# Kernel tuning notes

Hardware: AMD Instinct MI355X
Metric: run time of the kernel (lower is better)

Reference implementation:

```python
import jax, jax.numpy as jnp
import numpy as np

V, E, H = 32000, 256, 512

def gru_cell(x, h, W_ih, W_hh, b_ih, b_hh):
    # PyTorch GRU cell: gates ordered (r, z, n)
    gi = x @ W_ih.T + b_ih
    gh = h @ W_hh.T + b_hh
    i_r, i_z, i_n = jnp.split(gi, 3, axis=-1)
    h_r, h_z, h_n = jnp.split(gh, 3, axis=-1)
    r = jax.nn.sigmoid(i_r + h_r)
    z = jax.nn.sigmoid(i_z + h_z)
    n = jnp.tanh(i_n + r * h_n)
    return (1.0 - z) * n + z * h


def setup_inputs() -> dict:
    key = jax.random.key(0)
    ks = jax.random.split(key, 16)
    B, Tx, Ty = 32, 512, 128
    s = lambda k, sh: jax.random.normal(k, sh, jnp.float32) * 0.05
    return {
        "x": jax.random.randint(ks[0], (B, Tx), 0, V),
        "y": jax.random.randint(ks[1], (B, Ty), 0, V),
        "embedding": s(ks[2], (V, E)),
        "enc_W_ih": s(ks[3], (3 * H, E)),
        "enc_W_hh": s(ks[4], (3 * H, H)),
        "enc_b_ih": s(ks[5], (3 * H,)),
        "enc_b_hh": s(ks[6], (3 * H,)),
        "dec_W_ih": s(ks[7], (3 * H, E + H)),
        "dec_W_hh": s(ks[8], (3 * H, H)),
        "dec_b_ih": s(ks[9], (3 * H,)),
        "dec_b_hh": s(ks[10], (3 * H,)),
        "h_init": s(ks[11], (1, H)),
        "fc_W": s(ks[12], (V, H)),
        "fc_b": s(ks[13], (V,)),
    }


def reference(x, y, embedding, enc_W_ih, enc_W_hh, enc_b_ih, enc_b_hh,
              dec_W_ih, dec_W_hh, dec_b_ih, dec_b_hh, h_init, fc_W, fc_b):
    B = x.shape[0]
    # ---- encode ----
    ex = embedding[x]  # [B, Tx, E]
    def enc_step(h, xt):
        h2 = gru_cell(xt, h, enc_W_ih, enc_W_hh, enc_b_ih, enc_b_hh)
        return h2, h2
    h0 = jnp.zeros((B, H), ex.dtype)
    _, eh = jax.lax.scan(enc_step, h0, jnp.swapaxes(ex, 0, 1))
    eh = jnp.swapaxes(eh, 0, 1)  # [B, Tx, H]

    # ---- decode with per-step dot-product attention ----
    inputs = embedding[y[:, :-1]]  # [B, Ty-1, E]
    ox0 = jnp.broadcast_to(h_init, (B, H)).astype(ex.dtype)
    hx0 = jnp.zeros((B, H), ex.dtype)
    def dec_step(carry, it):
        ox, hx = carry
        scores = jnp.einsum('bth,bh->bt', eh, ox)       # dot-product attention
        a = jax.nn.softmax(scores, axis=1)              # softmax over time
        sx = jnp.einsum('bth,bt->bh', eh, a)            # context summary
        ix = jnp.concatenate([it, sx], axis=-1)         # [B, E+H]
        hx2 = gru_cell(ix, hx, dec_W_ih, dec_W_hh, dec_b_ih, dec_b_hh)
        return (hx2, hx2), hx2 + sx                     # ox = dec output = hx (1 layer)
    _, outs = jax.lax.scan(dec_step, (ox0, hx0), jnp.swapaxes(inputs, 0, 1))
    out = jnp.swapaxes(outs, 0, 1)  # [B, Ty-1, H]
    return out @ fc_W.T + fc_b      # [B, Ty-1, V]
```

## Files before the change

### kernel.cpp

```cpp
#include <hip/hip_runtime.h>
#include <hip/hip_bf16.h>


#define B_  32
#define TX_ 512
#define TY_ 127
#define E_  256
#define H_  512
#define G3_ 1536
#define V_  32000
#define NA_ 128
#define NW_ 32

typedef unsigned short u16;
typedef short short8 __attribute__((ext_vector_type(8)));
typedef float f32x4 __attribute__((ext_vector_type(4)));
typedef float f32x2 __attribute__((ext_vector_type(2)));
typedef unsigned int u32x4 __attribute__((ext_vector_type(4)));

__device__ __forceinline__ float bfu(u16 h){ union{unsigned u; float f;} x; x.u=((unsigned)h)<<16; return x.f; }
__device__ __forceinline__ u16 f2bf(float f){ union{float f; unsigned u;} v; v.f=f; unsigned r=v.u+0x7fffu+((v.u>>16)&1u); return (u16)(r>>16); }
__device__ __forceinline__ float sigm(float x){ return 1.f/(1.f+__expf(-x)); }
__device__ __forceinline__ float tanh_f(float x){ return 1.f - 2.f/(__expf(2.f*x)+1.f); }

__device__ __forceinline__ u32x4 ld16_c(const void* p){
  u32x4 r;
  asm volatile("global_load_dwordx4 %0, %1, off sc0 sc1\n\ts_waitcnt vmcnt(0)"
               : "=v"(r) : "v"(p) : "memory");
  return r;
}
__device__ __forceinline__ f32x2 ld8_c(const void* p){
  f32x2 r;
  asm volatile("global_load_dwordx2 %0, %1, off sc0 sc1\n\ts_waitcnt vmcnt(0)"
               : "=v"(r) : "v"(p) : "memory");
  return r;
}
__device__ __forceinline__ void ld3f_c(const float* p0, const float* p1, const float* p2,
                                       float& a, float& b, float& c){
  asm volatile(
    "global_load_dword %0, %3, off sc0 sc1\n\t"
    "global_load_dword %1, %4, off sc0 sc1\n\t"
    "global_load_dword %2, %5, off sc0 sc1\n\t"
    "s_waitcnt vmcnt(0)"
    : "=&v"(a),"=&v"(b),"=&v"(c)
    : "v"(p0),"v"(p1),"v"(p2) : "memory");
}
__device__ __forceinline__ void st_u16_c(void* p, unsigned v){
  asm volatile("global_store_short %0, %1, off sc0 sc1" :: "v"(p), "v"(v) : "memory");
}
__device__ __forceinline__ void st8_c(void* p, float a, float b){
  f32x2 v; v.x=a; v.y=b;
  asm volatile("global_store_dwordx2 %0, %1, off sc0 sc1" :: "v"(p), "v"(v) : "memory");
}
__device__ __forceinline__ void st4f_c(void* p, float v){
  asm volatile("global_store_dword %0, %1, off sc0 sc1" :: "v"(p), "v"(v) : "memory");
}

__device__ __forceinline__ void spin_rel(int* p, int tgt){
  int n = 0;
  while (__hip_atomic_load(p, __ATOMIC_RELAXED, __HIP_MEMORY_SCOPE_AGENT) < tgt){
    __builtin_amdgcn_s_sleep(1);
    if (++n > (1<<22)) break;
  }
}

__device__ __forceinline__ void flagbar(int* flags, int target){
  __syncthreads();
  if (threadIdx.x == 0)
    __hip_atomic_store(&flags[blockIdx.x], target, __ATOMIC_RELAXED, __HIP_MEMORY_SCOPE_AGENT);
  if (threadIdx.x < 32) spin_rel(&flags[threadIdx.x], target);
  __syncthreads();
  asm volatile("" ::: "memory");
}

__device__ __forceinline__ void stage4_c(u16 (*stgl)[520], const u16* src, int tid){
  const u16* b0 = src + (size_t)(tid>>6)*H_ + (tid&63)*8;
  const u16* b1 = b0 + (size_t)8*H_;
  const u16* b2 = b0 + (size_t)16*H_;
  const u16* b3 = b0 + (size_t)24*H_;
  u32x4 q0,q1,q2,q3;
  asm volatile(
    "global_load_dwordx4 %0, %4, off sc0 sc1\n\t"
    "global_load_dwordx4 %1, %5, off sc0 sc1\n\t"
    "global_load_dwordx4 %2, %6, off sc0 sc1\n\t"
    "global_load_dwordx4 %3, %7, off sc0 sc1\n\t"
    "s_waitcnt vmcnt(0)"
    : "=&v"(q0),"=&v"(q1),"=&v"(q2),"=&v"(q3)
    : "v"(b0),"v"(b1),"v"(b2),"v"(b3) : "memory");
  int r = tid>>6, c = (tid&63)*8;
  *(u32x4*)&stgl[r][c]    = q0;
  *(u32x4*)&stgl[r+8][c]  = q1;
  *(u32x4*)&stgl[r+16][c] = q2;
  *(u32x4*)&stgl[r+24][c] = q3;
}

__global__ void cvt_rows(const float* __restrict__ src, int sld, int soff,
                         u16* __restrict__ dst, int cols){
  int r = blockIdx.x;
  const float* s = src + (size_t)r*sld + soff;
  u16* d = dst + (size_t)r*cols;
  for (int c = threadIdx.x; c < cols; c += blockDim.x) d[c] = f2bf(s[c]);
}

__global__ void gather_embed(const float* __restrict__ emb, const int* __restrict__ idx,
                             u16* __restrict__ dst, int rows_per_b, int ld){
  int m = blockIdx.x;
  int bb = m / rows_per_b, tt = m - bb*rows_per_b;
  int id = idx[bb*ld + tt];
  dst[(size_t)m*E_ + threadIdx.x] = f2bf(emb[(size_t)id*E_ + threadIdx.x]);
}

__global__ __launch_bounds__(256) void gemm_bf16(
    const u16* __restrict__ A, int lda, const u16* __restrict__ Bm, int ldb,
    void* __restrict__ Cout, int ldc, const float* __restrict__ bias,
    int M, int K, int out_bf16)
{
  int wave = threadIdx.x >> 6, lane = threadIdx.x & 63;
  int m0 = blockIdx.x*128 + (wave>>1)*64;
  int n0 = blockIdx.y*128 + (wave&1)*64;
  int lr = lane & 15, lk = (lane>>4)*8;
  f32x4 acc[4][4];
  #pragma unroll
  for (int i=0;i<4;++i)
    #pragma unroll
    for (int j=0;j<4;++j) acc[i][j] = (f32x4){0.f,0.f,0.f,0.f};
  for (int k0=0; k0<K; k0+=32){
    short8 af[4], bfv[4];
    #pragma unroll
    for (int i=0;i<4;++i){
      int row = m0 + i*16 + lr; if (row > M-1) row = M-1;
      af[i] = *(const short8*)(A + (size_t)row*lda + k0 + lk);
    }
    #pragma unroll
    for (int j=0;j<4;++j){
      int col = n0 + j*16 + lr;
      bfv[j] = *(const short8*)(Bm + (size_t)col*ldb + k0 + lk);
    }
    #pragma unroll
    for (int i=0;i<4;++i)
      #pragma unroll
      for (int j=0;j<4;++j)
        acc[i][j] = __builtin_amdgcn_mfma_f32_16x16x32_bf16(af[i], bfv[j], acc[i][j], 0,0,0);
  }
  int rbase = (lane>>4)*4;
  #pragma unroll
  for (int i=0;i<4;++i)
    #pragma unroll
    for (int r=0;r<4;++r){
      int row = m0 + i*16 + rbase + r;
      if (row < M){
        #pragma unroll
        for (int j=0;j<4;++j){
          int col = n0 + j*16 + lr;
          float v = acc[i][j][r] + bias[col];
          if (out_bf16) ((u16*)Cout)[(size_t)row*ldc + col] = f2bf(v);
          else          ((float*)Cout)[(size_t)row*ldc + col] = v;
        }
      }
    }
}

__global__ __launch_bounds__(512,2) void enc_v2(
    const u16* __restrict__ Gx, const u16* __restrict__ Whh_bf,
    const float* __restrict__ bhh, u16* __restrict__ eh,
    u16* __restrict__ hgd, int* flags)
{
  __shared__ __align__(16) u16 stgl[32][520];
  __shared__ __align__(16) float gH[32][52];
  int tid = threadIdx.x, g = blockIdx.x;
  int wave = tid>>6, lane = tid&63;
  int pb = tid>>4, pu = tid&15, u = g*16 + pu;

  short8 fH[16];
  int mt = wave/3, nt = wave%3;
  if (wave < 6){
    int row = nt*H_ + g*16 + (lane&15);
    int kb = (lane>>4)*8;
    #pragma unroll
    for (int ks=0;ks<16;++ks)
      fH[ks] = *(const short8*)(Whh_bf + (size_t)row*H_ + ks*32 + kb);
  }
  float bhR = bhh[u], bhZ = bhh[u+H_], bhN = bhh[u+2*H_];
  float hloc = 0.f;

  for (int t=0;t<TX_;++t){
    size_t gxb = ((size_t)pb*TX_ + t)*G3_;
    float iR = bfu(Gx[gxb+u]), iZ = bfu(Gx[gxb+H_+u]), iN = bfu(Gx[gxb+2*H_+u]);
    stage4_c(stgl, hgd + (size_t)(t&1)*B_*H_, tid);
    __syncthreads();
    if (wave < 6){
      f32x4 acc = (f32x4){0.f,0.f,0.f,0.f};
      int ar = mt*16 + (lane&15), ak = (lane>>4)*8;
      #pragma unroll
      for (int ks=0;ks<16;++ks)
        acc = __builtin_amdgcn_mfma_f32_16x16x32_bf16(*(const short8*)&stgl[ar][ks*32+ak], fH[ks], acc, 0,0,0);
      int dr = mt*16 + ((lane>>4)<<2), dc = nt*16 + (lane&15);
      #pragma unroll
      for (int r=0;r<4;++r) gH[dr+r][dc] = acc[r];
    }
    __syncthreads();
    float r = sigm(iR + gH[pb][pu]    + bhR);
    float z = sigm(iZ + gH[pb][16+pu] + bhZ);
    float n = tanh_f(iN + r*(gH[pb][32+pu] + bhN));
    hloc = (1.f-z)*n + z*hloc;
    u16 hb = f2bf(hloc);
    st_u16_c(&hgd[(size_t)((t+1)&1)*B_*H_ + (size_t)pb*H_ + u], (unsigned)hb);
    eh[((size_t)pb*TX_ + t)*H_ + u] = hb;
    flagbar(flags, t+1);
  }
}

__global__ __launch_bounds__(512,2) void dec_v4(
    const u16* __restrict__ eh, const u16* __restrict__ Gy,
    const u16* __restrict__ WihS_bf, const u16* __restrict__ Whh_bf,
    const float* __restrict__ dbhh, const float* __restrict__ hinit,
    u16* __restrict__ sxb, u16* __restrict__ hdd2,
    float* __restrict__ part, float* __restrict__ statsg,
    u16* __restrict__ Xfc,
    int* Pf, int* Xf, int* Hf)
{
  struct AS {
    u16   ehq[128][512];
    u16   oxb[512];
    float sc[128];
    float pt[8][512];
    float red[16];
    float st4[8];
  };
  struct WS { u16 stgl[32][520]; float gS[32][52]; float gH[32][52]; };
  __shared__ __align__(16) char smem_[sizeof(AS)];
  int tid = threadIdx.x;
  int wave = tid>>6, lane = tid&63;

  if (blockIdx.x < NA_){
    AS& S = *(AS*)smem_;
    int b = blockIdx.x >> 2, q = blockIdx.x & 3;
    {
      const u16* ehg = eh + ((size_t)b*TX_ + q*128)*H_;
      int row = tid>>2, c0 = (tid&3)*128;
      #pragma unroll
      for (int j=0;j<16;++j){
        int u0 = c0 + j*8;
        uint4 v = *(const uint4*)(ehg + (size_t)row*H_ + u0);
        *(uint4*)&S.ehq[row][u0 ^ ((row&7)<<3)] = v;
      }
    }
    __syncthreads();
    bool bl = (lane&15) == 0;
    for (int t=0;t<TY_;++t){
      if (t > 0){
        if (tid < NW_) spin_rel(&Hf[tid], t);
        __syncthreads();
        asm volatile("" ::: "memory");
        if (tid < 64){
          u32x4 qv = ld16_c(hdd2 + (size_t)(t&1)*B_*H_ + (size_t)b*H_ + tid*8);
          *(u32x4*)&S.oxb[tid*8] = qv;
        }
      } else {
        S.oxb[tid] = f2bf(hinit[tid]);
      }
      __syncthreads();
      {
        f32x4 acS = (f32x4){0.f,0.f,0.f,0.f};
        int arow = wave*16 + (lane&15);
        int swz = (arow&7)<<3;
        #pragma unroll
        for (int kt=0;kt<16;++kt){
          short8 bf = (short8){0,0,0,0,0,0,0,0};
          if (bl) bf = *(const short8*)&S.oxb[kt*32 + (lane>>4)*8];
          short8 af_ = *(const short8*)&S.ehq[arow][(kt*32 + (lane>>4)*8) ^ swz];
          acS = __builtin_amdgcn_mfma_f32_16x16x32_bf16(af_, bf, acS, 0,0,0);
        }
        if (bl){
          #pragma unroll
          for (int r=0;r<4;++r) S.sc[wave*16 + (lane>>4)*4 + r] = acS[r];
        }
      }
      __syncthreads();
      float mq, lq;
      {
        float v = (tid<128) ? S.sc[tid] : -3e38f;
        #pragma unroll
        for (int o=32;o>0;o>>=1) v = fmaxf(v, __shfl_xor(v, o));
        if (lane==0) S.red[wave] = v;
        __syncthreads();
        mq = fmaxf(S.red[0], S.red[1]);
        float e = 0.f;
        if (tid<128){ e = __expf(S.sc[tid] - mq); S.sc[tid] = e; }
        float s2 = e;
        #pragma unroll
        for (int o=32;o>0;o>>=1) s2 += __shfl_xor(s2, o);
        if (lane==0) S.red[8+wave] = s2;
        __syncthreads();
        lq = S.red[8] + S.red[9];
      }
      int u0 = lane*8, tseg = wave;
      f32x4 aLo = (f32x4){0.f,0.f,0.f,0.f}, aHi = (f32x4){0.f,0.f,0.f,0.f};
      #pragma unroll
      for (int j=0;j<16;++j){
        int tp = tseg*16 + j;
        short8 ev = *(const short8*)&S.ehq[tp][u0 ^ ((tp&7)<<3)];
        float av = S.sc[tp];
        aLo[0] = fmaf(bfu((u16)ev[0]), av, aLo[0]);
        aLo[1] = fmaf(bfu((u16)ev[1]), av, aLo[1]);
        aLo[2] = fmaf(bfu((u16)ev[2]), av, aLo[2]);
        aLo[3] = fmaf(bfu((u16)ev[3]), av, aLo[3]);
        aHi[0] = fmaf(bfu((u16)ev[4]), av, aHi[0]);
        aHi[1] = fmaf(bfu((u16)ev[5]), av, aHi[1]);
        aHi[2] = fmaf(bfu((u16)ev[6]), av, aHi[2]);
        aHi[3] = fmaf(bfu((u16)ev[7]), av, aHi[3]);
      }
      *(f32x4*)&S.pt[tseg][u0]   = aLo;
      *(f32x4*)&S.pt[tseg][u0+4] = aHi;
      __syncthreads();
      float sv = 0.f;
      #pragma unroll
      for (int gsg=0; gsg<8; ++gsg) sv += S.pt[gsg][tid];
      if (q != 0){
        st4f_c(&part[(size_t)(b*4+q)*512 + tid], sv);
        if (tid==0) st8_c(&statsg[(size_t)(b*4+q)*2], mq, lq);
        __syncthreads();
        if (tid==0) __hip_atomic_store(&Pf[b*4+q], t+1, __ATOMIC_RELAXED, __HIP_MEMORY_SCOPE_AGENT);
      } else {
        if (tid < 3) spin_rel(&Pf[b*4+1+tid], t+1);
        __syncthreads();
        asm volatile("" ::: "memory");
        if (tid < 3){
          f32x2 r2 = ld8_c(&statsg[(size_t)(b*4+1+tid)*2]);
          S.st4[tid*2] = r2.x; S.st4[tid*2+1] = r2.y;
        }
        __syncthreads();
        float m1=S.st4[0], l1=S.st4[1], m2=S.st4[2], l2=S.st4[3], m3=S.st4[4], l3=S.st4[5];
        float gmax = fmaxf(fmaxf(mq,m1), fmaxf(m2,m3));
        float e0=__expf(mq-gmax), e1=__expf(m1-gmax), e2=__expf(m2-gmax), e3=__expf(m3-gmax);
        float inv = 1.f/(lq*e0 + l1*e1 + l2*e2 + l3*e3);
        float p1,p2,p3;
        ld3f_c(&part[(size_t)(b*4+1)*512 + tid], &part[(size_t)(b*4+2)*512 + tid],
               &part[(size_t)(b*4+3)*512 + tid], p1, p2, p3);
        float sx = (sv*e0 + p1*e1 + p2*e2 + p3*e3) * inv;
        st_u16_c(&sxb[(size_t)b*H_ + tid], (unsigned)f2bf(sx));
        __syncthreads();
        if (tid==0) __hip_atomic_store(&Xf[b], t+1, __ATOMIC_RELAXED, __HIP_MEMORY_SCOPE_AGENT);
      }
    }
  } else {
    WS& S = *(WS*)smem_;
    int g = blockIdx.x - NA_;
    int pb = tid>>4, pu = tid&15, u = g*16 + pu;
    short8 fS[16], fH[16];
    int mt = wave/3, nt = wave%3;
    if (wave < 6){
      int row = nt*H_ + g*16 + (lane&15);
      int kb = (lane>>4)*8;
      #pragma unroll
      for (int ks=0;ks<16;++ks){
        fS[ks] = *(const short8*)(WihS_bf + (size_t)row*H_ + ks*32 + kb);
        fH[ks] = *(const short8*)(Whh_bf  + (size_t)row*H_ + ks*32 + kb);
      }
    }
    float bhR = dbhh[u], bhZ = dbhh[u+H_], bhN = dbhh[u+2*H_];
    float hloc = 0.f;

    for (int t=0;t<TY_;++t){
      size_t gyb = ((size_t)pb*TY_ + t)*G3_;
      float iR = bfu(Gy[gyb+u]), iZ = bfu(Gy[gyb+H_+u]), iN = bfu(Gy[gyb+2*H_+u]);
      if (tid < NW_) spin_rel(&Hf[tid], t);
      __syncthreads();
      asm volatile("" ::: "memory");
      stage4_c(S.stgl, hdd2 + (size_t)(t&1)*B_*H_, tid);
      __syncthreads();
      int ar = mt*16 + (lane&15), ak = (lane>>4)*8;
      if (wave < 6){
        f32x4 acc = (f32x4){0.f,0.f,0.f,0.f};
        #pragma unroll
        for (int ks=0;ks<16;++ks)
          acc = __builtin_amdgcn_mfma_f32_16x16x32_bf16(*(const short8*)&S.stgl[ar][ks*32+ak], fH[ks], acc, 0,0,0);
        int dr = mt*16 + ((lane>>4)<<2), dc = nt*16 + (lane&15);
        #pragma unroll
        for (int r=0;r<4;++r) S.gH[dr+r][dc] = acc[r];
      }
      if (tid < 32) spin_rel(&Xf[tid], t+1);
      __syncthreads();
      asm volatile("" ::: "memory");
      stage4_c(S.stgl, sxb, tid);
      __syncthreads();
      float sxv = bfu(S.stgl[pb][u]);
      if (wave < 6){
        f32x4 acc = (f32x4){0.f,0.f,0.f,0.f};
        #pragma unroll
        for (int ks=0;ks<16;++ks)
          acc = __builtin_amdgcn_mfma_f32_16x16x32_bf16(*(const short8*)&S.stgl[ar][ks*32+ak], fS[ks], acc, 0,0,0);
        int dr = mt*16 + ((lane>>4)<<2), dc = nt*16 + (lane&15);
        #pragma unroll
        for (int r=0;r<4;++r) S.gS[dr+r][dc] = acc[r];
      }
      __syncthreads();
      {
        float r = sigm(iR + S.gS[pb][pu]    + S.gH[pb][pu]    + bhR);
        float z = sigm(iZ + S.gS[pb][16+pu] + S.gH[pb][16+pu] + bhZ);
        float n = tanh_f(iN + S.gS[pb][32+pu] + r*(S.gH[pb][32+pu] + bhN));
        hloc = (1.f-z)*n + z*hloc;
        st_u16_c(&hdd2[(size_t)((t+1)&1)*B_*H_ + (size_t)pb*H_ + u], (unsigned)f2bf(hloc));
        Xfc[((size_t)pb*TY_ + t)*H_ + u] = f2bf(hloc + sxv);
      }
      __syncthreads();
      if (tid==0) __hip_atomic_store(&Hf[g], t+1, __ATOMIC_RELAXED, __HIP_MEMORY_SCOPE_AGENT);
    }
  }
}

extern "C" void kernel_launch(void* const* d_in, const int* in_sizes, int n_in,
                              void* d_out, int out_size, void* d_ws, size_t ws_size,
                              hipStream_t stream) {
  const int*   x     = (const int*)d_in[0];
  const int*   y     = (const int*)d_in[1];
  const float* emb   = (const float*)d_in[2];
  const float* eWih  = (const float*)d_in[3];
  const float* eWhh  = (const float*)d_in[4];
  const float* eBih  = (const float*)d_in[5];
  const float* eBhh  = (const float*)d_in[6];
  const float* dWih  = (const float*)d_in[7];
  const float* dWhh  = (const float*)d_in[8];
  const float* dBih  = (const float*)d_in[9];
  const float* dBhh  = (const float*)d_in[10];
  const float* hinit = (const float*)d_in[11];
  const float* fcW   = (const float*)d_in[12];
  const float* fcB   = (const float*)d_in[13];
  float* out = (float*)d_out;
  (void)in_sizes; (void)n_in; (void)out_size; (void)ws_size;

  char* p = (char*)d_ws;
  auto take = [&](size_t bytes)->char*{ char* r = p; p += (bytes + 255) & ~(size_t)255; return r; };
  u16* Wfc_bf   = (u16*)take((size_t)V_*H_*2);
  u16* ex_bf    = (u16*)take((size_t)B_*TX_*E_*2);
  u16* eWih_bf  = (u16*)take((size_t)G3_*E_*2);
  u16* Gx_bf    = (u16*)take((size_t)B_*TX_*G3_*2);
  u16* eh_bf    = (u16*)take((size_t)B_*TX_*H_*2);
  u16* embY_bf  = (u16*)take((size_t)4096*E_*2);
  u16* dWihE_bf = (u16*)take((size_t)G3_*E_*2);
  u16* Gy_bf    = (u16*)take((size_t)4096*G3_*2);
  u16* Xfc_bf   = (u16*)take((size_t)4096*H_*2);
  u16* eWhh_bf  = (u16*)take((size_t)G3_*H_*2);
  u16* dWhh_bf  = (u16*)take((size_t)G3_*H_*2);
  u16* dWihS_bf = (u16*)take((size_t)G3_*H_*2);
  u16* hgd      = (u16*)take((size_t)2*B_*H_*2);
  u16* hdd2     = (u16*)take((size_t)2*B_*H_*2);
  u16* sxb      = (u16*)take((size_t)B_*H_*2);
  float* part   = (float*)take((size_t)NA_*H_*4);
  float* statsg = (float*)take((size_t)NA_*2*4);
  int* flagsE   = (int*)take(256);
  int* ctrl     = (int*)take(4096);
  int* Pf = ctrl, *Xf = ctrl+128, *Hf = ctrl+160;

  hipMemsetAsync(flagsE, 0, 256, stream);
  hipMemsetAsync(ctrl, 0, 4096, stream);
  hipMemsetAsync(hgd, 0, (size_t)2*B_*H_*2, stream);
  hipMemsetAsync(hdd2, 0, (size_t)2*B_*H_*2, stream);

  cvt_rows<<<dim3(V_),  dim3(256), 0, stream>>>(fcW,  H_, 0, Wfc_bf,   H_);
  cvt_rows<<<dim3(G3_), dim3(256), 0, stream>>>(eWih, E_, 0, eWih_bf,  E_);
  cvt_rows<<<dim3(G3_), dim3(256), 0, stream>>>(dWih, E_+H_, 0, dWihE_bf, E_);
  cvt_rows<<<dim3(G3_), dim3(256), 0, stream>>>(eWhh, H_, 0, eWhh_bf,  H_);
  cvt_rows<<<dim3(G3_), dim3(256), 0, stream>>>(dWhh, H_, 0, dWhh_bf,  H_);
  cvt_rows<<<dim3(G3_), dim3(256), 0, stream>>>(dWih, E_+H_, E_, dWihS_bf, H_);

  gather_embed<<<dim3(B_*TX_), dim3(E_), 0, stream>>>(emb, x, ex_bf, TX_, TX_);
  gather_embed<<<dim3(B_*TY_), dim3(E_), 0, stream>>>(emb, y, embY_bf, TY_, 128);

  gemm_bf16<<<dim3(B_*TX_/128, G3_/128), dim3(256), 0, stream>>>(
      ex_bf, E_, eWih_bf, E_, Gx_bf, G3_, eBih, B_*TX_, E_, 1);
  gemm_bf16<<<dim3(32, G3_/128), dim3(256), 0, stream>>>(
      embY_bf, E_, dWihE_bf, E_, Gy_bf, G3_, dBih, B_*TY_, E_, 1);

  enc_v2<<<dim3(32), dim3(512), 0, stream>>>(Gx_bf, eWhh_bf, eBhh, eh_bf, hgd, flagsE);

  dec_v4<<<dim3(NA_+NW_), dim3(512), 0, stream>>>(eh_bf, Gy_bf, dWihS_bf, dWhh_bf,
                                                  dBhh, hinit, sxb, hdd2, part, statsg,
                                                  Xfc_bf, Pf, Xf, Hf);

  gemm_bf16<<<dim3(32, V_/128), dim3(256), 0, stream>>>(
      Xfc_bf, H_, Wfc_bf, H_, out, V_, fcB, B_*TY_, H_, 0);
}
```

Measured before the change: 3.293 ms.

## Fuse output projection into decoder kernel with ticketed overlap; loosen encoder barrier

```diff
diff --git a/kernel.cpp b/kernel.cpp
--- a/kernel.cpp
+++ b/kernel.cpp
@@ -11,6 +11,7 @@
 #define V_  32000
 #define NA_ 128
 #define NW_ 32
+#define NF_ 80
 
 typedef unsigned short u16;
 typedef short short8 __attribute__((ext_vector_type(8)));
@@ -28,22 +29,6 @@
   asm volatile("global_load_dwordx4 %0, %1, off sc0 sc1\n\ts_waitcnt vmcnt(0)"
                : "=v"(r) : "v"(p) : "memory");
   return r;
-}
-__device__ __forceinline__ f32x2 ld8_c(const void* p){
-  f32x2 r;
-  asm volatile("global_load_dwordx2 %0, %1, off sc0 sc1\n\ts_waitcnt vmcnt(0)"
-               : "=v"(r) : "v"(p) : "memory");
-  return r;
-}
-__device__ __forceinline__ void ld3f_c(const float* p0, const float* p1, const float* p2,
-                                       float& a, float& b, float& c){
-  asm volatile(
-    "global_load_dword %0, %3, off sc0 sc1\n\t"
-    "global_load_dword %1, %4, off sc0 sc1\n\t"
-    "global_load_dword %2, %5, off sc0 sc1\n\t"
-    "s_waitcnt vmcnt(0)"
-    : "=&v"(a),"=&v"(b),"=&v"(c)
-    : "v"(p0),"v"(p1),"v"(p2) : "memory");
 }
 __device__ __forceinline__ void st_u16_c(void* p, unsigned v){
   asm volatile("global_store_short %0, %1, off sc0 sc1" :: "v"(p), "v"(v) : "memory");
@@ -63,14 +48,12 @@
     if (++n > (1<<22)) break;
   }
 }
-
-__device__ __forceinline__ void flagbar(int* flags, int target){
-  __syncthreads();
-  if (threadIdx.x == 0)
-    __hip_atomic_store(&flags[blockIdx.x], target, __ATOMIC_RELAXED, __HIP_MEMORY_SCOPE_AGENT);
-  if (threadIdx.x < 32) spin_rel(&flags[threadIdx.x], target);
-  __syncthreads();
-  asm volatile("" ::: "memory");
+__device__ __forceinline__ void spin_rel_slow(int* p, int tgt){
+  int n = 0;
+  while (__hip_atomic_load(p, __ATOMIC_RELAXED, __HIP_MEMORY_SCOPE_AGENT) < tgt){
+    __builtin_amdgcn_s_sleep(16);
+    if (++n > (1<<20)) break;
+  }
 }
 
 __device__ __forceinline__ void stage4_c(u16 (*stgl)[520], const u16* src, int tid){
@@ -160,7 +143,7 @@
     }
 }
 
-__global__ __launch_bounds__(512,2) void enc_v2(
+__global__ __launch_bounds__(512,2) void enc_v3(
     const u16* __restrict__ Gx, const u16* __restrict__ Whh_bf,
     const float* __restrict__ bhh, u16* __restrict__ eh,
     u16* __restrict__ hgd, int* flags)
@@ -182,10 +165,15 @@
   }
   float bhR = bhh[u], bhZ = bhh[u+H_], bhN = bhh[u+2*H_];
   float hloc = 0.f;
+  size_t gx0 = (size_t)pb*TX_*G3_;
+  float iR = bfu(Gx[gx0+u]), iZ = bfu(Gx[gx0+H_+u]), iN = bfu(Gx[gx0+2*H_+u]);
 
   for (int t=0;t<TX_;++t){
-    size_t gxb = ((size_t)pb*TX_ + t)*G3_;
-    float iR = bfu(Gx[gxb+u]), iZ = bfu(Gx[gxb+H_+u]), iN = bfu(Gx[gxb+2*H_+u]);
+    if (t > 0){
+      if (tid < 32) spin_rel(&flags[tid], t);
+      __syncthreads();
+      asm volatile("" ::: "memory");
+    }
     stage4_c(stgl, hgd + (size_t)(t&1)*B_*H_, tid);
     __syncthreads();
     if (wave < 6){
@@ -205,19 +193,26 @@
     hloc = (1.f-z)*n + z*hloc;
     u16 hb = f2bf(hloc);
     st_u16_c(&hgd[(size_t)((t+1)&1)*B_*H_ + (size_t)pb*H_ + u], (unsigned)hb);
+    __syncthreads();
+    if (tid == 0)
+      __hip_atomic_store(&flags[blockIdx.x], t+1, __ATOMIC_RELAXED, __HIP_MEMORY_SCOPE_AGENT);
     eh[((size_t)pb*TX_ + t)*H_ + u] = hb;
-    flagbar(flags, t+1);
+    if (t+1 < TX_){
+      size_t g2 = ((size_t)pb*TX_ + (t+1))*G3_;
+      iR = bfu(Gx[g2+u]); iZ = bfu(Gx[g2+H_+u]); iN = bfu(Gx[g2+2*H_+u]);
+    }
   }
 }
 
-__global__ __launch_bounds__(512,2) void dec_v4(
+__global__ __launch_bounds__(512,2) void dec_v5(
     const u16* __restrict__ eh, const u16* __restrict__ Gy,
     const u16* __restrict__ WihS_bf, const u16* __restrict__ Whh_bf,
     const float* __restrict__ dbhh, const float* __restrict__ hinit,
+    const u16* __restrict__ Wfc_bf, const float* __restrict__ fcB,
     u16* __restrict__ sxb, u16* __restrict__ hdd2,
     float* __restrict__ part, float* __restrict__ statsg,
-    u16* __restrict__ Xfc,
-    int* Pf, int* Xf, int* Hf)
+    u16* __restrict__ XfcT, float* __restrict__ out,
+    int* Pf, int* Xf, int* Hf, int* ticket)
 {
   struct AS {
     u16   ehq[128][512];
@@ -225,9 +220,9 @@
     float sc[128];
     float pt[8][512];
     float red[16];
-    float st4[8];
   };
   struct WS { u16 stgl[32][520]; float gS[32][52]; float gH[32][52]; };
+  struct FS { u16 Ab[128][520]; int tkS; };
   __shared__ __align__(16) char smem_[sizeof(AS)];
   int tid = threadIdx.x;
   int wave = tid>>6, lane = tid&63;
@@ -325,25 +320,35 @@
         if (tid < 3) spin_rel(&Pf[b*4+1+tid], t+1);
         __syncthreads();
         asm volatile("" ::: "memory");
-        if (tid < 3){
-          f32x2 r2 = ld8_c(&statsg[(size_t)(b*4+1+tid)*2]);
-          S.st4[tid*2] = r2.x; S.st4[tid*2+1] = r2.y;
-        }
-        __syncthreads();
-        float m1=S.st4[0], l1=S.st4[1], m2=S.st4[2], l2=S.st4[3], m3=S.st4[4], l3=S.st4[5];
-        float gmax = fmaxf(fmaxf(mq,m1), fmaxf(m2,m3));
-        float e0=__expf(mq-gmax), e1=__expf(m1-gmax), e2=__expf(m2-gmax), e3=__expf(m3-gmax);
-        float inv = 1.f/(lq*e0 + l1*e1 + l2*e2 + l3*e3);
-        float p1,p2,p3;
-        ld3f_c(&part[(size_t)(b*4+1)*512 + tid], &part[(size_t)(b*4+2)*512 + tid],
-               &part[(size_t)(b*4+3)*512 + tid], p1, p2, p3);
+        float p1,p2,p3; f32x2 s1,s2,s3;
+        {
+          const float* pp1 = &part[(size_t)(b*4+1)*512 + tid];
+          const float* pp2 = &part[(size_t)(b*4+2)*512 + tid];
+          const float* pp3 = &part[(size_t)(b*4+3)*512 + tid];
+          const float* ps1 = &statsg[(size_t)(b*4+1)*2];
+          const float* ps2 = &statsg[(size_t)(b*4+2)*2];
+          const float* ps3 = &statsg[(size_t)(b*4+3)*2];
+          asm volatile(
+            "global_load_dword %0, %6, off sc0 sc1\n\t"
+            "global_load_dword %1, %7, off sc0 sc1\n\t"
+            "global_load_dword %2, %8, off sc0 sc1\n\t"
+            "global_load_dwordx2 %3, %9, off sc0 sc1\n\t"
+            "global_load_dwordx2 %4, %10, off sc0 sc1\n\t"
+            "global_load_dwordx2 %5, %11, off sc0 sc1\n\t"
+            "s_waitcnt vmcnt(0)"
+            : "=&v"(p1),"=&v"(p2),"=&v"(p3),"=&v"(s1),"=&v"(s2),"=&v"(s3)
+            : "v"(pp1),"v"(pp2),"v"(pp3),"v"(ps1),"v"(ps2),"v"(ps3) : "memory");
+        }
+        float gmax = fmaxf(fmaxf(mq,s1.x), fmaxf(s2.x,s3.x));
+        float e0=__expf(mq-gmax), e1=__expf(s1.x-gmax), e2=__expf(s2.x-gmax), e3=__expf(s3.x-gmax);
+        float inv = 1.f/(lq*e0 + s1.y*e1 + s2.y*e2 + s3.y*e3);
         float sx = (sv*e0 + p1*e1 + p2*e2 + p3*e3) * inv;
         st_u16_c(&sxb[(size_t)b*H_ + tid], (unsigned)f2bf(sx));
         __syncthreads();
         if (tid==0) __hip_atomic_store(&Xf[b], t+1, __ATOMIC_RELAXED, __HIP_MEMORY_SCOPE_AGENT);
       }
     }
-  } else {
+  } else if (blockIdx.x < NA_ + NW_){
     WS& S = *(WS*)smem_;
     int g = blockIdx.x - NA_;
     int pb = tid>>4, pu = tid&15, u = g*16 + pu;
@@ -401,10 +406,78 @@
         float n = tanh_f(iN + S.gS[pb][32+pu] + r*(S.gH[pb][32+pu] + bhN));
         hloc = (1.f-z)*n + z*hloc;
         st_u16_c(&hdd2[(size_t)((t+1)&1)*B_*H_ + (size_t)pb*H_ + u], (unsigned)f2bf(hloc));
-        Xfc[((size_t)pb*TY_ + t)*H_ + u] = f2bf(hloc + sxv);
+        st_u16_c(&XfcT[((size_t)t*B_ + pb)*H_ + u], (unsigned)f2bf(hloc + sxv));
       }
       __syncthreads();
       if (tid==0) __hip_atomic_store(&Hf[g], t+1, __ATOMIC_RELAXED, __HIP_MEMORY_SCOPE_AGENT);
+    }
+  } else {
+    FS& S = *(FS*)smem_;
+    int lr = lane & 15, lk = (lane>>4)*8;
+    int m0 = (wave>>2)*64, n0w = (wave&3)*64;
+    while (true){
+      if (tid == 0)
+        S.tkS = __hip_atomic_fetch_add(ticket, 1, __ATOMIC_RELAXED, __HIP_MEMORY_SCOPE_AGENT);
+      __syncthreads();
+      int tk = S.tkS;
+      __syncthreads();
+      if (tk >= 32*32) break;
+      int tb = tk >> 5, c = tk & 31;
+      int nbase = c*4;
+      int nbend = (nbase+4 < 125) ? nbase+4 : 125;
+      int te = 4*tb + 4; if (te > TY_) te = TY_;
+      if (tid < NW_) spin_rel_slow(&Hf[tid], te);
+      __syncthreads();
+      asm volatile("" ::: "memory");
+      {
+        const u16* src = XfcT + (size_t)tb*128*H_;
+        #pragma unroll
+        for (int it2=0; it2<16; ++it2){
+          int el = (it2*512 + tid)*8;
+          int rr = el >> 9, cc = el & 511;
+          u32x4 v = ld16_c(src + (size_t)rr*H_ + cc);
+          *(u32x4*)&S.Ab[rr][cc] = v;
+        }
+      }
+      __syncthreads();
+      for (int nb = nbase; nb < nbend; ++nb){
+        int ncol0 = nb*256 + n0w;
+        f32x4 acc[4][4];
+        #pragma unroll
+        for (int i=0;i<4;++i)
+          #pragma unroll
+          for (int j=0;j<4;++j) acc[i][j] = (f32x4){0.f,0.f,0.f,0.f};
+        for (int k0=0; k0<H_; k0+=32){
+          short8 af[4], bfv[4];
+          #pragma unroll
+          for (int i=0;i<4;++i)
+            af[i] = *(const short8*)&S.Ab[m0 + i*16 + lr][k0 + lk];
+          #pragma unroll
+          for (int j=0;j<4;++j)
+            bfv[j] = *(const short8*)(Wfc_bf + (size_t)(ncol0 + j*16 + lr)*H_ + k0 + lk);
+          #pragma unroll
+          for (int i=0;i<4;++i)
+            #pragma unroll
+            for (int j=0;j<4;++j)
+              acc[i][j] = __builtin_amdgcn_mfma_f32_16x16x32_bf16(af[i], bfv[j], acc[i][j], 0,0,0);
+        }
+        int rbase = (lane>>4)*4;
+        #pragma unroll
+        for (int i=0;i<4;++i)
+          #pragma unroll
+          for (int r=0;r<4;++r){
+            int arow = m0 + i*16 + rbase + r;
+            int t2 = tb*4 + (arow>>5), b2 = arow&31;
+            if (t2 < TY_){
+              #pragma unroll
+              for (int j=0;j<4;++j){
+                int col = ncol0 + j*16 + lr;
+                out[((size_t)b2*TY_ + t2)*V_ + col] = acc[i][j][r] + fcB[col];
+              }
+            }
+          }
+        __syncthreads();
+      }
     }
   }
 }
@@ -439,7 +512,7 @@
   u16* embY_bf  = (u16*)take((size_t)4096*E_*2);
   u16* dWihE_bf = (u16*)take((size_t)G3_*E_*2);
   u16* Gy_bf    = (u16*)take((size_t)4096*G3_*2);
-  u16* Xfc_bf   = (u16*)take((size_t)4096*H_*2);
+  u16* XfcT_bf  = (u16*)take((size_t)4096*H_*2);
   u16* eWhh_bf  = (u16*)take((size_t)G3_*H_*2);
   u16* dWhh_bf  = (u16*)take((size_t)G3_*H_*2);
   u16* dWihS_bf = (u16*)take((size_t)G3_*H_*2);
@@ -450,7 +523,7 @@
   float* statsg = (float*)take((size_t)NA_*2*4);
   int* flagsE   = (int*)take(256);
   int* ctrl     = (int*)take(4096);
-  int* Pf = ctrl, *Xf = ctrl+128, *Hf = ctrl+160;
+  int* Pf = ctrl, *Xf = ctrl+128, *Hf = ctrl+160, *ticket = ctrl+200;
 
   hipMemsetAsync(flagsE, 0, 256, stream);
   hipMemsetAsync(ctrl, 0, 4096, stream);
@@ -472,12 +545,9 @@
   gemm_bf16<<<dim3(32, G3_/128), dim3(256), 0, stream>>>(
       embY_bf, E_, dWihE_bf, E_, Gy_bf, G3_, dBih, B_*TY_, E_, 1);
 
-  enc_v2<<<dim3(32), dim3(512), 0, stream>>>(Gx_bf, eWhh_bf, eBhh, eh_bf, hgd, flagsE);
-
-  dec_v4<<<dim3(NA_+NW_), dim3(512), 0, stream>>>(eh_bf, Gy_bf, dWihS_bf, dWhh_bf,
-                                                  dBhh, hinit, sxb, hdd2, part, statsg,
-                                                  Xfc_bf, Pf, Xf, Hf);
-
-  gemm_bf16<<<dim3(32, V_/128), dim3(256), 0, stream>>>(
-      Xfc_bf, H_, Wfc_bf, H_, out, V_, fcB, B_*TY_, H_, 0);
-}
+  enc_v3<<<dim3(32), dim3(512), 0, stream>>>(Gx_bf, eWhh_bf, eBhh, eh_bf, hgd, flagsE);
+
+  dec_v5<<<dim3(NA_+NW_+NF_), dim3(512), 0, stream>>>(
+      eh_bf, Gy_bf, dWihS_bf, dWhh_bf, dBhh, hinit, Wfc_bf, fcB,
+      sxb, hdd2, part, statsg, XfcT_bf, out, Pf, Xf, Hf, ticket);
+}
```

After: 2.684 ms. 18.5% less time.
